# Kernel optimization log

Hardware: AMD Instinct MI355X
Metric: run time of the kernel (lower is better)

The kernel has to match this reference:

```python
import jax, jax.numpy as jnp
import numpy as np

EXTENTS = (1, 1, 1)
DIM = 256
HEADS = 8
DH = 32
INNER = HEADS * DH
SCALE = DH ** -0.5
NEG = -1e9


def _windows(t):
    """t: (B, S, H, W, C) -> (B, S, H, W, K, C) local 3D windows, K = prod(2e+1).
    Pads with zeros, window dims flattened in (s, h, w) order (matches unfold i j k)."""
    e = EXTENTS
    B, S, H, W, C = t.shape
    tp = jnp.pad(t, [(0, 0), (e[0], e[0]), (e[1], e[1]), (e[2], e[2]), (0, 0)])
    slabs = []
    for dz in range(2 * e[0] + 1):
        for dy in range(2 * e[1] + 1):
            for dx in range(2 * e[2] + 1):
                slabs.append(tp[:, dz:dz + S, dy:dy + H, dx:dx + W, :])
    return jnp.stack(slabs, axis=4)


def setup_inputs() -> dict:
    key = jax.random.key(0)
    ks = jax.random.split(key, 8)
    B, S, H, W = 2, 8, 32, 32
    scale_w = DIM ** -0.5
    return {
        "x": jax.random.normal(ks[0], (B, S, H, W, DIM), jnp.float32),
        "q": jax.random.normal(ks[1], (B, S, H, W, DIM), jnp.float32),
        "Wq": jax.random.normal(ks[2], (DIM, INNER), jnp.float32) * scale_w,
        "Wk": jax.random.normal(ks[3], (DIM, INNER), jnp.float32) * scale_w,
        "Wv": jax.random.normal(ks[4], (DIM, INNER), jnp.float32) * scale_w,
        "bv": jax.random.normal(ks[5], (INNER,), jnp.float32) * 0.02,
        "Wo": jax.random.normal(ks[6], (INNER, DIM), jnp.float32) * (INNER ** -0.5),
        "bo": jax.random.normal(ks[7], (DIM,), jnp.float32) * 0.02,
    }


def reference(x, q, Wq, Wk, Wv, bv, Wo, bo):
    B, S, H, W, _ = x.shape
    k = x @ Wk                      # (B,S,H,W,INNER)
    v = x @ Wv + bv
    qp = q @ Wq

    kw = _windows(k)                # (B,S,H,W,K,INNER)
    vw = _windows(v)
    K = kw.shape[4]

    # mask: True where window element falls on padding (out of bounds)
    valid = _windows(jnp.ones((1, S, H, W, 1), jnp.float32))[..., 0] > 0  # (1,S,H,W,K)
    mask = ~valid

    qh = qp.reshape(B, S, H, W, HEADS, DH)
    kh = kw.reshape(B, S, H, W, K, HEADS, DH)
    vh = vw.reshape(B, S, H, W, K, HEADS, DH)

    dots = jnp.einsum('bshwnd,bshwknd->bshwnk', qh, kh) * SCALE  # (B,S,H,W,HEADS,K)
    dots = jnp.where(mask[:, :, :, :, None, :], NEG, dots)
    attn = jax.nn.softmax(dots, axis=-1)
    out = jnp.einsum('bshwnk,bshwknd->bshwnd', attn, vh)
    out = out.reshape(B, S, H, W, INNER)
    return out @ Wo + bo            # (B,S,H,W,DIM)
```

## Files before the change

### kernel.cpp

```cpp
#include <hip/hip_runtime.h>
#include <hip/hip_bf16.h>
#include <math.h>

#define B_N 2
#define S_N 8
#define H_N 32
#define W_N 32
#define DIM_N 256
#define NPOS (B_N * S_N * H_N * W_N)
#define NP (NPOS * DIM_N)
#define SCALE_F 0.1767766952966369f

typedef __attribute__((ext_vector_type(8))) short bf16x8;
typedef __attribute__((ext_vector_type(4))) float f32x4;

__device__ __forceinline__ unsigned short f2b(float f) {
    __hip_bfloat16 h = __float2bfloat16(f);
    return __builtin_bit_cast(unsigned short, h);
}
__device__ __forceinline__ unsigned pk2(float a, float b) {
    return (unsigned)f2b(a) | ((unsigned)f2b(b) << 16);
}
__device__ __forceinline__ float bl(unsigned u) { return __uint_as_float(u << 16); }
__device__ __forceinline__ float bh(unsigned u) { return __uint_as_float(u & 0xffff0000u); }

__global__ __launch_bounds__(256)
void wtrans_kernel(const float* __restrict__ Wq, const float* __restrict__ Wk,
                   const float* __restrict__ Wv, const float* __restrict__ Wo,
                   unsigned short* __restrict__ wt)
{
    int mat = blockIdx.y;
    const float* W = (mat == 0) ? Wq : (mat == 1) ? Wk : (mat == 2) ? Wv : Wo;
    unsigned short* Wt = wt + (size_t)mat * 65536;
    int tile = blockIdx.x;
    int tk = tile >> 3, tn = tile & 7;
    __shared__ float t[32][33];
    int c = threadIdx.x & 31;
    int r0 = (threadIdx.x >> 5) * 4;
#pragma unroll
    for (int i = 0; i < 4; ++i)
        t[r0 + i][c] = W[(size_t)(tk * 32 + r0 + i) * 256 + tn * 32 + c];
    __syncthreads();
#pragma unroll
    for (int i = 0; i < 4; ++i)
        Wt[(size_t)(tn * 32 + r0 + i) * 256 + tk * 32 + c] = f2b(t[c][r0 + i]);
}

__global__ __launch_bounds__(512, 4)
void proj_mfma(const float* __restrict__ x, const float* __restrict__ q,
               const unsigned short* __restrict__ wt, const float* __restrict__ bv,
               unsigned short* __restrict__ qh, unsigned short* __restrict__ kh,
               unsigned short* __restrict__ vh)
{
    __shared__ unsigned short Al[64][72];
    __shared__ unsigned short Bl[256][72];

    const int bx = blockIdx.x;
    const int z = bx >> 8;
    const int row0 = (bx & 255) * 64;
    const float* A = (z == 0) ? q : x;
    const unsigned short* Wtm = wt + (size_t)z * 65536;
    unsigned short* outp = (z == 0) ? qh : (z == 1) ? kh : vh;
    const float* bias = (z == 2) ? bv : nullptr;

    const int tid = threadIdx.x;
    const int lane = tid & 63;
    const int wid = tid >> 6;
    const int wm = wid >> 2, wn = wid & 3;
    const int l15 = lane & 15, l4 = lane >> 4;

    f32x4 acc[2][4];
#pragma unroll
    for (int m = 0; m < 2; ++m)
#pragma unroll
        for (int n = 0; n < 4; ++n) acc[m][n] = (f32x4){0.f, 0.f, 0.f, 0.f};

    const int ar = tid >> 3, as = tid & 7;

    for (int kt = 0; kt < DIM_N; kt += 64) {
        {
            const float* p = &A[(size_t)(row0 + ar) * DIM_N + kt + as * 8];
            float4 f0 = *(const float4*)p;
            float4 f1 = *(const float4*)(p + 4);
            uint4 va;
            va.x = pk2(f0.x, f0.y); va.y = pk2(f0.z, f0.w);
            va.z = pk2(f1.x, f1.y); va.w = pk2(f1.z, f1.w);
            *(uint4*)&Al[ar][as * 8] = va;
        }
#pragma unroll
        for (int i = 0; i < 4; ++i) {
            int u = tid + i * 512;
            int rowb = u >> 3, su = u & 7;
            *(uint4*)&Bl[rowb][su * 8] =
                *(const uint4*)&Wtm[(size_t)rowb * DIM_N + kt + su * 8];
        }
        __syncthreads();
#pragma unroll
        for (int ks = 0; ks < 2; ++ks) {
            bf16x8 af[2], bfr[4];
#pragma unroll
            for (int m = 0; m < 2; ++m)
                af[m] = *(const bf16x8*)&Al[wm * 32 + m * 16 + l15][ks * 32 + l4 * 8];
#pragma unroll
            for (int n = 0; n < 4; ++n)
                bfr[n] = *(const bf16x8*)&Bl[wn * 64 + n * 16 + l15][ks * 32 + l4 * 8];
#pragma unroll
            for (int m = 0; m < 2; ++m)
#pragma unroll
                for (int n = 0; n < 4; ++n)
                    acc[m][n] = __builtin_amdgcn_mfma_f32_16x16x32_bf16(
                        af[m], bfr[n], acc[m][n], 0, 0, 0);
        }
        __syncthreads();
    }

#pragma unroll
    for (int n = 0; n < 4; ++n) {
        int col = wn * 64 + n * 16 + l15;
        float bb = bias ? bias[col] : 0.f;
        int head = col >> 5, dh = col & 31;
#pragma unroll
        for (int m = 0; m < 2; ++m) {
#pragma unroll
            for (int rg = 0; rg < 4; ++rg) {
                int row = row0 + wm * 32 + m * 16 + l4 * 4 + rg;
                outp[((size_t)head * NPOS + row) * 32 + dh] =
                    f2b(acc[m][n][rg] + bb);
            }
        }
    }
}

__global__ __launch_bounds__(256, 2)
void attn_fused(const unsigned short* __restrict__ qh, const unsigned short* __restrict__ kh,
                const unsigned short* __restrict__ vh, const unsigned short* __restrict__ wt3,
                const float* __restrict__ bo, float* __restrict__ out)
{
    __shared__ unsigned short aol[32 * 256];
    __shared__ unsigned short Bl[256][72];

    int p = blockIdx.x;
    int bix = (p & 7) * 64 + (p >> 3);
    int h = bix & 31, s = (bix >> 5) & 7, b = bix >> 8;
    int n = threadIdx.x >> 5;
    int w = threadIdx.x & 31;

    size_t rowbase = (((size_t)b * S_N + s) * H_N + h) * W_N;
    size_t pos = rowbase + w;
    const unsigned short* qrow = qh + ((size_t)n * NPOS + pos) * 32;
    float qv[32];
#pragma unroll
    for (int j = 0; j < 4; ++j) {
        uint4 u = ((const uint4*)qrow)[j];
        qv[j * 8 + 0] = bl(u.x); qv[j * 8 + 1] = bh(u.x);
        qv[j * 8 + 2] = bl(u.y); qv[j * 8 + 3] = bh(u.y);
        qv[j * 8 + 4] = bl(u.z); qv[j * 8 + 5] = bh(u.z);
        qv[j * 8 + 6] = bl(u.w); qv[j * 8 + 7] = bh(u.w);
    }

    float dots[27];
#pragma unroll
    for (int dz = 0; dz < 3; ++dz)
#pragma unroll
        for (int dy = 0; dy < 3; ++dy) {
            int ns = s + dz - 1, nh = h + dy - 1;
            bool rowok = (unsigned)ns < S_N && (unsigned)nh < H_N;
            size_t rb = rowok ? ((((size_t)b * S_N + ns) * H_N + nh) * W_N)
                              : rowbase;
            const unsigned short* base = kh + ((size_t)n * NPOS + rb + w) * 32;
            uint4 kr[3][4];
#pragma unroll
            for (int dx = 0; dx < 3; ++dx) {
                const uint4* kp = (const uint4*)(base + (dx - 1) * 32);
#pragma unroll
                for (int j = 0; j < 4; ++j) kr[dx][j] = kp[j];
            }
#pragma unroll
            for (int dx = 0; dx < 3; ++dx) {
                float acc = 0.f;
#pragma unroll
                for (int j = 0; j < 4; ++j) {
                    uint4 u = kr[dx][j];
                    acc = fmaf(qv[j * 8 + 0], bl(u.x), acc);
                    acc = fmaf(qv[j * 8 + 1], bh(u.x), acc);
                    acc = fmaf(qv[j * 8 + 2], bl(u.y), acc);
                    acc = fmaf(qv[j * 8 + 3], bh(u.y), acc);
                    acc = fmaf(qv[j * 8 + 4], bl(u.z), acc);
                    acc = fmaf(qv[j * 8 + 5], bh(u.z), acc);
                    acc = fmaf(qv[j * 8 + 6], bl(u.w), acc);
                    acc = fmaf(qv[j * 8 + 7], bh(u.w), acc);
                }
                int nw = w + dx - 1;
                bool ok = rowok && (unsigned)nw < W_N;
                dots[(dz * 3 + dy) * 3 + dx] = ok ? acc * SCALE_F : -1e30f;
            }
        }

    float m = dots[0];
#pragma unroll
    for (int i = 1; i < 27; ++i) m = fmaxf(m, dots[i]);
    float den = 0.f;
#pragma unroll
    for (int i = 0; i < 27; ++i) {
        float p2 = __expf(dots[i] - m);
        dots[i] = p2;
        den += p2;
    }
    float inv = 1.f / den;

    float ov[32];
#pragma unroll
    for (int i = 0; i < 32; ++i) ov[i] = 0.f;
#pragma unroll
    for (int dz = 0; dz < 3; ++dz)
#pragma unroll
        for (int dy = 0; dy < 3; ++dy) {
            int ns = s + dz - 1, nh = h + dy - 1;
            bool rowok = (unsigned)ns < S_N && (unsigned)nh < H_N;
            size_t rb = rowok ? ((((size_t)b * S_N + ns) * H_N + nh) * W_N)
                              : rowbase;
            const unsigned short* base = vh + ((size_t)n * NPOS + rb + w) * 32;
            uint4 vr[3][4];
#pragma unroll
            for (int dx = 0; dx < 3; ++dx) {
                const uint4* vp = (const uint4*)(base + (dx - 1) * 32);
#pragma unroll
                for (int j = 0; j < 4; ++j) vr[dx][j] = vp[j];
            }
#pragma unroll
            for (int dx = 0; dx < 3; ++dx) {
                float pw = dots[(dz * 3 + dy) * 3 + dx];
#pragma unroll
                for (int j = 0; j < 4; ++j) {
                    uint4 u = vr[dx][j];
                    ov[j * 8 + 0] = fmaf(pw, bl(u.x), ov[j * 8 + 0]);
                    ov[j * 8 + 1] = fmaf(pw, bh(u.x), ov[j * 8 + 1]);
                    ov[j * 8 + 2] = fmaf(pw, bl(u.y), ov[j * 8 + 2]);
                    ov[j * 8 + 3] = fmaf(pw, bh(u.y), ov[j * 8 + 3]);
                    ov[j * 8 + 4] = fmaf(pw, bl(u.z), ov[j * 8 + 4]);
                    ov[j * 8 + 5] = fmaf(pw, bh(u.z), ov[j * 8 + 5]);
                    ov[j * 8 + 6] = fmaf(pw, bl(u.w), ov[j * 8 + 6]);
                    ov[j * 8 + 7] = fmaf(pw, bh(u.w), ov[j * 8 + 7]);
                }
            }
        }

#pragma unroll
    for (int j = 0; j < 4; ++j) {
        uint4 o;
        o.x = pk2(ov[j * 8 + 0] * inv, ov[j * 8 + 1] * inv);
        o.y = pk2(ov[j * 8 + 2] * inv, ov[j * 8 + 3] * inv);
        o.z = pk2(ov[j * 8 + 4] * inv, ov[j * 8 + 5] * inv);
        o.w = pk2(ov[j * 8 + 6] * inv, ov[j * 8 + 7] * inv);
        int unit = n * 4 + j;
        int su = unit ^ (w & 7);
        *(uint4*)&aol[w * 256 + su * 8] = o;
    }

    const int lane = threadIdx.x & 63;
    const int wv = threadIdx.x >> 6;
    const int l15 = lane & 15, l4 = lane >> 4;

    f32x4 acc[2][4];
#pragma unroll
    for (int m2 = 0; m2 < 2; ++m2)
#pragma unroll
        for (int n2 = 0; n2 < 4; ++n2) acc[m2][n2] = (f32x4){0.f, 0.f, 0.f, 0.f};

    for (int kt = 0; kt < 4; ++kt) {
        __syncthreads();
#pragma unroll
        for (int i = 0; i < 8; ++i) {
            int u = threadIdx.x + i * 256;
            int rowb = u >> 3, su = u & 7;
            *(uint4*)&Bl[rowb][su * 8] =
                *(const uint4*)&wt3[(size_t)rowb * DIM_N + kt * 64 + su * 8];
        }
        __syncthreads();
#pragma unroll
        for (int ks = 0; ks < 2; ++ks) {
            bf16x8 af[2], bfr[4];
#pragma unroll
            for (int m2 = 0; m2 < 2; ++m2) {
                int r = m2 * 16 + l15;
                int unit = kt * 8 + ks * 4 + l4;
                int su = unit ^ (r & 7);
                af[m2] = *(const bf16x8*)&aol[r * 256 + su * 8];
            }
#pragma unroll
            for (int n2 = 0; n2 < 4; ++n2)
                bfr[n2] = *(const bf16x8*)&Bl[wv * 64 + n2 * 16 + l15][ks * 32 + l4 * 8];
#pragma unroll
            for (int m2 = 0; m2 < 2; ++m2)
#pragma unroll
                for (int n2 = 0; n2 < 4; ++n2)
                    acc[m2][n2] = __builtin_amdgcn_mfma_f32_16x16x32_bf16(
                        af[m2], bfr[n2], acc[m2][n2], 0, 0, 0);
        }
    }

#pragma unroll
    for (int n2 = 0; n2 < 4; ++n2) {
        int col = wv * 64 + n2 * 16 + l15;
        float bb = bo[col];
#pragma unroll
        for (int m2 = 0; m2 < 2; ++m2) {
#pragma unroll
            for (int rg = 0; rg < 4; ++rg) {
                int row = m2 * 16 + l4 * 4 + rg;
                out[(rowbase + row) * DIM_N + col] = acc[m2][n2][rg] + bb;
            }
        }
    }
}

extern "C" void kernel_launch(void* const* d_in, const int* in_sizes, int n_in,
                              void* d_out, int out_size, void* d_ws, size_t ws_size,
                              hipStream_t stream)
{
    const float* xin = (const float*)d_in[0];
    const float* qin = (const float*)d_in[1];
    const float* Wq  = (const float*)d_in[2];
    const float* Wk  = (const float*)d_in[3];
    const float* Wv  = (const float*)d_in[4];
    const float* bv  = (const float*)d_in[5];
    const float* Wo  = (const float*)d_in[6];
    const float* bo  = (const float*)d_in[7];
    float* out = (float*)d_out;

    unsigned short* ws = (unsigned short*)d_ws;
    unsigned short* wt = ws;
    unsigned short* qh = wt + (size_t)4 * 65536;
    unsigned short* kh = qh + (size_t)NP;
    unsigned short* vh = kh + (size_t)NP;

    dim3 gw(64, 4);
    wtrans_kernel<<<gw, 256, 0, stream>>>(Wq, Wk, Wv, Wo, wt);

    proj_mfma<<<768, 512, 0, stream>>>(xin, qin, wt, bv, qh, kh, vh);

    attn_fused<<<B_N * S_N * H_N, 256, 0, stream>>>(qh, kh, vh, wt + 3 * 65536, bo, out);
}
```

Measured before the change: 63.58 us.

## Retile projection GEMM to 128x128 tiles with direct global-to-LDS weight loads

```diff
diff --git a/kernel.cpp b/kernel.cpp
--- a/kernel.cpp
+++ b/kernel.cpp
@@ -46,18 +46,20 @@
         Wt[(size_t)(tn * 32 + r0 + i) * 256 + tk * 32 + c] = f2b(t[c][r0 + i]);
 }
 
-__global__ __launch_bounds__(512, 4)
+__global__ __launch_bounds__(256, 3)
 void proj_mfma(const float* __restrict__ x, const float* __restrict__ q,
                const unsigned short* __restrict__ wt, const float* __restrict__ bv,
                unsigned short* __restrict__ qh, unsigned short* __restrict__ kh,
                unsigned short* __restrict__ vh)
 {
-    __shared__ unsigned short Al[64][72];
-    __shared__ unsigned short Bl[256][72];
+    __shared__ unsigned short Al[128][72];
+    __shared__ unsigned short Bl[128][64];
 
     const int bx = blockIdx.x;
     const int z = bx >> 8;
-    const int row0 = (bx & 255) * 64;
+    const int rem = bx & 255;
+    const int row0 = (rem >> 1) * 128;
+    const int col0 = (rem & 1) * 128;
     const float* A = (z == 0) ? q : x;
     const unsigned short* Wtm = wt + (size_t)z * 65536;
     unsigned short* outp = (z == 0) ? qh : (z == 1) ? kh : vh;
@@ -66,46 +68,54 @@
     const int tid = threadIdx.x;
     const int lane = tid & 63;
     const int wid = tid >> 6;
-    const int wm = wid >> 2, wn = wid & 3;
+    const int wr = wid >> 1, wc = wid & 1;
     const int l15 = lane & 15, l4 = lane >> 4;
 
-    f32x4 acc[2][4];
-#pragma unroll
-    for (int m = 0; m < 2; ++m)
+    f32x4 acc[4][4];
+#pragma unroll
+    for (int m = 0; m < 4; ++m)
 #pragma unroll
         for (int n = 0; n < 4; ++n) acc[m][n] = (f32x4){0.f, 0.f, 0.f, 0.f};
 
-    const int ar = tid >> 3, as = tid & 7;
-
     for (int kt = 0; kt < DIM_N; kt += 64) {
-        {
-            const float* p = &A[(size_t)(row0 + ar) * DIM_N + kt + as * 8];
-            float4 f0 = *(const float4*)p;
-            float4 f1 = *(const float4*)(p + 4);
-            uint4 va;
-            va.x = pk2(f0.x, f0.y); va.y = pk2(f0.z, f0.w);
-            va.z = pk2(f1.x, f1.y); va.w = pk2(f1.z, f1.w);
-            *(uint4*)&Al[ar][as * 8] = va;
-        }
 #pragma unroll
         for (int i = 0; i < 4; ++i) {
-            int u = tid + i * 512;
-            int rowb = u >> 3, su = u & 7;
-            *(uint4*)&Bl[rowb][su * 8] =
-                *(const uint4*)&Wtm[(size_t)rowb * DIM_N + kt + su * 8];
+            int c = wid * 4 + i;
+            int o = c * 64 + lane;
+            int row = o >> 3, u = o & 7;
+            int lu = u ^ (row & 7);
+            const unsigned short* g =
+                &Wtm[(size_t)(col0 + row) * DIM_N + kt + lu * 8];
+            __builtin_amdgcn_global_load_lds(
+                (const __attribute__((address_space(1))) unsigned int*)g,
+                (__attribute__((address_space(3))) unsigned int*)&Bl[c * 8][0],
+                16, 0, 0);
+        }
+#pragma unroll
+        for (int i = 0; i < 8; ++i) {
+            int o = i * 256 + tid;
+            int row = o >> 4, qq = o & 15;
+            float4 f = *(const float4*)&A[(size_t)(row0 + row) * DIM_N + kt + qq * 4];
+            uint2 v;
+            v.x = pk2(f.x, f.y);
+            v.y = pk2(f.z, f.w);
+            *(uint2*)&Al[row][qq * 4] = v;
         }
         __syncthreads();
 #pragma unroll
         for (int ks = 0; ks < 2; ++ks) {
-            bf16x8 af[2], bfr[4];
-#pragma unroll
-            for (int m = 0; m < 2; ++m)
-                af[m] = *(const bf16x8*)&Al[wm * 32 + m * 16 + l15][ks * 32 + l4 * 8];
-#pragma unroll
-            for (int n = 0; n < 4; ++n)
-                bfr[n] = *(const bf16x8*)&Bl[wn * 64 + n * 16 + l15][ks * 32 + l4 * 8];
-#pragma unroll
-            for (int m = 0; m < 2; ++m)
+            bf16x8 af[4], bfr[4];
+#pragma unroll
+            for (int m = 0; m < 4; ++m)
+                af[m] = *(const bf16x8*)&Al[wr * 64 + m * 16 + l15][ks * 32 + l4 * 8];
+#pragma unroll
+            for (int n = 0; n < 4; ++n) {
+                int row = wc * 64 + n * 16 + l15;
+                int su = (ks * 4 + l4) ^ (row & 7);
+                bfr[n] = *(const bf16x8*)&Bl[row][su * 8];
+            }
+#pragma unroll
+            for (int m = 0; m < 4; ++m)
 #pragma unroll
                 for (int n = 0; n < 4; ++n)
                     acc[m][n] = __builtin_amdgcn_mfma_f32_16x16x32_bf16(
@@ -116,14 +126,14 @@
 
 #pragma unroll
     for (int n = 0; n < 4; ++n) {
-        int col = wn * 64 + n * 16 + l15;
+        int col = col0 + wc * 64 + n * 16 + l15;
         float bb = bias ? bias[col] : 0.f;
         int head = col >> 5, dh = col & 31;
 #pragma unroll
-        for (int m = 0; m < 2; ++m) {
+        for (int m = 0; m < 4; ++m) {
 #pragma unroll
             for (int rg = 0; rg < 4; ++rg) {
-                int row = row0 + wm * 32 + m * 16 + l4 * 4 + rg;
+                int row = row0 + wr * 64 + m * 16 + l4 * 4 + rg;
                 outp[((size_t)head * NPOS + row) * 32 + dh] =
                     f2b(acc[m][n][rg] + bb);
             }
@@ -337,7 +347,7 @@
     dim3 gw(64, 4);
     wtrans_kernel<<<gw, 256, 0, stream>>>(Wq, Wk, Wv, Wo, wt);
 
-    proj_mfma<<<768, 512, 0, stream>>>(xin, qin, wt, bv, qh, kh, vh);
+    proj_mfma<<<768, 256, 0, stream>>>(xin, qin, wt, bv, qh, kh, vh);
 
     attn_fused<<<B_N * S_N * H_N, 256, 0, stream>>>(qh, kh, vh, wt + 3 * 65536, bo, out);
 }
```

Result: faster. 62.10 us (-2.3%).
